# Performance work log

Hardware: AMD Instinct MI355X
Metric: run time of the kernel (lower is better)

Reference implementation:

```python
import jax, jax.numpy as jnp
import numpy as np

PATCH_NUMS = (1, 2, 4, 8, 16)
BETA = 0.25
A = -0.75  # torch bicubic coefficient


def _cubic(s):
    s = abs(s)
    if s <= 1.0:
        return ((A + 2.0) * s - (A + 3.0)) * s * s + 1.0
    if s < 2.0:
        return (((s - 5.0) * s + 8.0) * s - 4.0) * A
    return 0.0


def bicubic_matrix(n_in, n_out):
    # Row-stochastic 1D resampling matrix matching torch upsample_bicubic2d
    # (align_corners=False: half-pixel centers, border index clamping).
    scale = n_in / n_out
    W = np.zeros((n_out, n_in), dtype=np.float32)
    for i in range(n_out):
        x = (i + 0.5) * scale - 0.5
        x0 = int(np.floor(x))
        t = x - x0
        for off in (-1, 0, 1, 2):
            idx = min(max(x0 + off, 0), n_in - 1)
            W[i, idx] += _cubic(t - off)
    return jnp.asarray(W)


def area_down(x, pn):
    # exact average pooling (h, w divisible by pn)
    b, c, h, w = x.shape
    kh, kw = h // pn, w // pn
    return x.reshape(b, c, pn, kh, pn, kw).mean(axis=(3, 5))


def bicubic_up(x, h_out, w_out):
    b, c, h_in, w_in = x.shape
    Wh = bicubic_matrix(h_in, h_out)  # (h_out, h_in)
    Ww = bicubic_matrix(w_in, w_out)  # (w_out, w_in)
    x = jnp.einsum('Oh,bchw->bcOw', Wh, x)
    x = jnp.einsum('Pw,bchw->bchP', Ww, x)
    return x


def vector_quantize(z, embed, beta):
    # z: (b,c,h,w); embed: (V,c)
    b, c, h, w = z.shape
    zf = z.transpose(0, 2, 3, 1).reshape(-1, c)  # (N,c)
    # squared L2 distances to codebook, (N,V)
    d = (zf * zf).sum(-1, keepdims=True) - 2.0 * zf @ embed.T + (embed * embed).sum(-1)
    idx = jnp.argmin(d, axis=1)  # (N,)
    zq = embed[idx].reshape(b, h, w, c).transpose(0, 3, 1, 2)
    sg = jax.lax.stop_gradient
    loss = beta * jnp.mean((sg(zq) - z) ** 2) + jnp.mean((zq - sg(z)) ** 2)
    zq_st = z + sg(zq - z)  # straight-through estimator
    return zq_st, idx.reshape(b, h, w), loss


def setup_inputs() -> dict:
    key = jax.random.key(0)
    k1, k2 = jax.random.split(key)
    z = jax.random.normal(k1, (256, 32, 16, 16), dtype=jnp.float32)
    embed = jax.random.normal(k2, (4096, 32), dtype=jnp.float32)
    return {"z": z, "embed": embed}


def reference(z, embed):
    b, c, h, w = z.shape
    f_rest = z
    f_hat = jnp.zeros_like(z)
    ms_idx = []
    vq_loss = jnp.float32(0.0)
    n = len(PATCH_NUMS)
    for i, pn in enumerate(PATCH_NUMS):
        z_scale = area_down(f_rest, pn) if i < n - 1 else f_rest
        z_q_scale, idx, loss_i = vector_quantize(z_scale, embed, BETA)
        z_q = bicubic_up(z_q_scale, h, w) if i < n - 1 else z_q_scale
        f_hat = f_hat + z_q
        f_rest = f_rest - z_q
        ms_idx.append(idx)
        vq_loss = vq_loss + loss_i
    vq_loss = vq_loss / n
    return (f_hat, *ms_idx, vq_loss)
```

## Files before the change

kernel.cpp:

```cpp
#include <hip/hip_runtime.h>
#include <hip/hip_bf16.h>
#include <cstdint>
#include <cstddef>


#define B_   256
#define V_   4096
#define NTOT 2097152
#define WIN  128
#define CAP  768

using bf16x8 = __attribute__((ext_vector_type(8))) short;
using f32x4  = __attribute__((ext_vector_type(4))) float;

__device__ inline short f2bf(float f) {
  __hip_bfloat16 h = __float2bfloat16(f);
  return *reinterpret_cast<short*>(&h);
}
__device__ inline unsigned encf(float f) {
  unsigned u = __float_as_uint(f);
  return (u & 0x80000000u) ? ~u : (u | 0x80000000u);
}
__device__ inline float decf(unsigned u) {
  unsigned b = (u & 0x80000000u) ? (u ^ 0x80000000u) : ~u;
  return __uint_as_float(b);
}
__device__ inline int keyidx(unsigned long long k) {
  int i = (int)(unsigned)(k & 0xffffffffull);
  return min(max(i, 0), V_ - 1);
}

__global__ __launch_bounds__(256) void setup_kernel(
    const float* __restrict__ z, const float* __restrict__ embed,
    float* __restrict__ f_rest, float* __restrict__ f_hat,
    float* __restrict__ zpack, short* __restrict__ ebf,
    float* __restrict__ se, float* __restrict__ tables,
    float* __restrict__ loss_slots, unsigned long long* __restrict__ keys0,
    unsigned int* __restrict__ smin0)
{
  const int tid = threadIdx.x;
  const int t = blockIdx.x * 256 + tid;
  float v = z[t];
  f_rest[t] = v;
  f_hat[t] = 0.f;

  __shared__ float sm[256];
  sm[tid] = v;
  __syncthreads();
  if (tid == 0) {
    float s = 0.f;
    for (int i = 0; i < 256; ++i) s += sm[i];
    zpack[blockIdx.x] = s * (1.0f / 256.0f);
  }

  if (blockIdx.x < 16) {
    int code = blockIdx.x * 256 + tid;
    float s = 0.f;
#pragma unroll
    for (int c = 0; c < 32; ++c) {
      float e = embed[(size_t)code * 32 + c];
      ebf[(size_t)code * 32 + c] = f2bf(e);
      s += e * e;
    }
    se[code] = s;
  } else if (blockIdx.x == 16) {
    if (tid < 64) {
      int pn_i = tid >> 4;
      int o    = tid & 15;
      int pn   = 1 << pn_i;
      double scale = (double)pn / 16.0;
      double x  = (o + 0.5) * scale - 0.5;
      double x0 = floor(x);
      double tf = x - x0;
      float row[8];
#pragma unroll
      for (int h = 0; h < 8; ++h) row[h] = 0.f;
      const double A = -0.75;
#pragma unroll
      for (int off = -1; off <= 2; ++off) {
        double s = fabs(tf - (double)off);
        double cub;
        if (s <= 1.0)      cub = ((A + 2.0) * s - (A + 3.0)) * s * s + 1.0;
        else if (s < 2.0)  cub = (((s - 5.0) * s + 8.0) * s - 4.0) * A;
        else               cub = 0.0;
        int idx = (int)x0 + off;
        idx = min(max(idx, 0), pn - 1);
        row[idx] = (float)((double)row[idx] + cub);
      }
#pragma unroll
      for (int h = 0; h < 8; ++h) tables[pn_i * 128 + o * 8 + h] = row[h];
    }
  } else if (blockIdx.x == 17) {
    keys0[tid] = ~0ull;
    smin0[tid] = 0xFFFFFFFFu;
  } else if (blockIdx.x >= 20 && blockIdx.x < 60) {
    loss_slots[(blockIdx.x - 20) * 256 + tid] = 0.f;
  }
}

__global__ __launch_bounds__(256) void vq_phaseA_kernel(
    const float* __restrict__ zpack, const short* __restrict__ ebf,
    const float* __restrict__ se, unsigned int* __restrict__ smin,
    int vchunk)
{
  __shared__ __align__(16) short elds[WIN * 40];
  __shared__ float selds[WIN];

  const int tid = threadIdx.x;
  const int lane = tid & 63, wave = tid >> 6;
  const int col = lane & 15, quad = lane >> 4;
  const int nw = blockIdx.x * 256 + wave * 64;
  const int vbase = blockIdx.y * vchunk;

  bf16x8 af[4];
#pragma unroll
  for (int f = 0; f < 4; ++f) {
    const float* zr = zpack + (size_t)(nw + f * 16 + col) * 32 + quad * 8;
    float4 x = *(const float4*)zr;
    float4 y = *(const float4*)(zr + 4);
    af[f] = bf16x8{f2bf(-x.x), f2bf(-x.y), f2bf(-x.z), f2bf(-x.w),
                   f2bf(-y.x), f2bf(-y.y), f2bf(-y.z), f2bf(-y.w)};
  }
  float mn[4][4];
#pragma unroll
  for (int f = 0; f < 4; ++f)
#pragma unroll
    for (int r = 0; r < 4; ++r) mn[f][r] = 3.4e38f;

  for (int w0 = 0; w0 < vchunk; w0 += WIN) {
    __syncthreads();
    {
      int row = tid >> 1, half = tid & 1;
      const bf16x8* src = (const bf16x8*)(ebf + (size_t)(vbase + w0 + row) * 32);
      bf16x8* dst = (bf16x8*)(elds + row * 40);
      dst[half * 2]     = src[half * 2];
      dst[half * 2 + 1] = src[half * 2 + 1];
      if (tid < WIN) selds[tid] = 0.5f * se[vbase + w0 + tid];
    }
    __syncthreads();
    for (int vv = 0; vv < WIN; vv += 16) {
      bf16x8 bf = *(const bf16x8*)(elds + (vv + col) * 40 + quad * 8);
      float sevh = selds[vv + col];
      f32x4 cin = {sevh, sevh, sevh, sevh};
#pragma unroll
      for (int f = 0; f < 4; ++f) {
        f32x4 d = __builtin_amdgcn_mfma_f32_16x16x32_bf16(af[f], bf, cin, 0, 0, 0);
#pragma unroll
        for (int r = 0; r < 4; ++r) mn[f][r] = fminf(mn[f][r], d[r]);
      }
    }
  }
#pragma unroll
  for (int f = 0; f < 4; ++f)
#pragma unroll
    for (int r = 0; r < 4; ++r) {
      float m = mn[f][r];
      m = fminf(m, __shfl_xor(m, 1, 64));
      m = fminf(m, __shfl_xor(m, 2, 64));
      m = fminf(m, __shfl_xor(m, 4, 64));
      m = fminf(m, __shfl_xor(m, 8, 64));
      mn[f][r] = m;
    }
  if (col == 0) {
#pragma unroll
    for (int f = 0; f < 4; ++f)
#pragma unroll
      for (int r = 0; r < 4; ++r)
        atomicMin(&smin[nw + f * 16 + quad * 4 + r], encf(mn[f][r]));
  }
}

__global__ __launch_bounds__(256) void vq_phaseB_kernel(
    const float* __restrict__ zpack, const short* __restrict__ ebf,
    const float* __restrict__ se, const unsigned int* __restrict__ smin,
    const float* __restrict__ embed, unsigned long long* __restrict__ keys,
    int vchunk, int nmax)
{
  __shared__ __align__(16) short elds[WIN * 40];
  __shared__ float selds[WIN];
  __shared__ unsigned long long clist[CAP];
  __shared__ int ccnt;

  const int tid = threadIdx.x;
  const int lane = tid & 63, wave = tid >> 6;
  const int col = lane & 15, quad = lane >> 4;
  const int nw = blockIdx.x * 256 + wave * 64;
  const int vbase = blockIdx.y * vchunk;
  const float MARGIN = 1.0f;

  if (tid == 0) ccnt = 0;
  __syncthreads();

  bf16x8 af[4];
#pragma unroll
  for (int f = 0; f < 4; ++f) {
    const float* zr = zpack + (size_t)(nw + f * 16 + col) * 32 + quad * 8;
    float4 x = *(const float4*)zr;
    float4 y = *(const float4*)(zr + 4);
    af[f] = bf16x8{f2bf(-x.x), f2bf(-x.y), f2bf(-x.z), f2bf(-x.w),
                   f2bf(-y.x), f2bf(-y.y), f2bf(-y.z), f2bf(-y.w)};
  }
  float thr[4][4];
#pragma unroll
  for (int f = 0; f < 4; ++f)
#pragma unroll
    for (int r = 0; r < 4; ++r)
      thr[f][r] = decf(smin[nw + f * 16 + quad * 4 + r]) + MARGIN;

  for (int w0 = 0; w0 < vchunk; w0 += WIN) {
    __syncthreads();
    {
      int row = tid >> 1, half = tid & 1;
      const bf16x8* src = (const bf16x8*)(ebf + (size_t)(vbase + w0 + row) * 32);
      bf16x8* dst = (bf16x8*)(elds + row * 40);
      dst[half * 2]     = src[half * 2];
      dst[half * 2 + 1] = src[half * 2 + 1];
      if (tid < WIN) selds[tid] = 0.5f * se[vbase + w0 + tid];
    }
    __syncthreads();
    for (int vv = 0; vv < WIN; vv += 16) {
      bf16x8 bf = *(const bf16x8*)(elds + (vv + col) * 40 + quad * 8);
      float sevh = selds[vv + col];
      f32x4 cin = {sevh, sevh, sevh, sevh};
      f32x4 dd[4];
      float hm = 3.4e38f;
#pragma unroll
      for (int f = 0; f < 4; ++f) {
        dd[f] = __builtin_amdgcn_mfma_f32_16x16x32_bf16(af[f], bf, cin, 0, 0, 0);
#pragma unroll
        for (int r = 0; r < 4; ++r) hm = fminf(hm, dd[f][r] - thr[f][r]);
      }
      if (hm <= 0.f) {
#pragma unroll
        for (int f = 0; f < 4; ++f) {
#pragma unroll
          for (int r = 0; r < 4; ++r) {
            if (dd[f][r] <= thr[f][r]) {
              int n = nw + f * 16 + quad * 4 + r;
              int v = vbase + w0 + vv + col;
              int slot = atomicAdd(&ccnt, 1);
              if (slot < CAP) {
                clist[slot] =
                    ((unsigned long long)(unsigned)n << 32) | (unsigned)v;
              } else {
                const float* zp = zpack + (size_t)n * 32;
                const float* ep = embed + (size_t)v * 32;
                float dot = 0.f, sz = 0.f;
#pragma unroll 1
                for (int i = 0; i < 8; ++i) {
                  float4 z4 = *(const float4*)(zp + 4 * i);
                  float4 e4 = *(const float4*)(ep + 4 * i);
                  dot = fmaf(z4.x, e4.x, dot); dot = fmaf(z4.y, e4.y, dot);
                  dot = fmaf(z4.z, e4.z, dot); dot = fmaf(z4.w, e4.w, dot);
                  sz  = fmaf(z4.x, z4.x, sz);  sz  = fmaf(z4.y, z4.y, sz);
                  sz  = fmaf(z4.z, z4.z, sz);  sz  = fmaf(z4.w, z4.w, sz);
                }
                float d = fmaf(-2.0f, dot, sz) + se[v];
                unsigned long long key =
                    ((unsigned long long)encf(d) << 32) | (unsigned)v;
                atomicMin(&keys[n], key);
              }
            }
          }
        }
      }
    }
  }

  __syncthreads();
  int tot = min(ccnt, CAP);
  for (int j = tid; j < tot; j += 256) {
    unsigned long long cv = clist[j];
    int n = min((int)(cv >> 32), nmax - 1);
    int v = min((int)(cv & 0xffffffffull), V_ - 1);
    const float* zp = zpack + (size_t)n * 32;
    const float* ep = embed + (size_t)v * 32;
    float dot = 0.f, sz = 0.f;
#pragma unroll
    for (int i = 0; i < 8; ++i) {
      float4 z4 = *(const float4*)(zp + 4 * i);
      float4 e4 = *(const float4*)(ep + 4 * i);
      dot = fmaf(z4.x, e4.x, dot); dot = fmaf(z4.y, e4.y, dot);
      dot = fmaf(z4.z, e4.z, dot); dot = fmaf(z4.w, e4.w, dot);
      sz  = fmaf(z4.x, z4.x, sz);  sz  = fmaf(z4.y, z4.y, sz);
      sz  = fmaf(z4.z, z4.z, sz);  sz  = fmaf(z4.w, z4.w, sz);
    }
    float d = fmaf(-2.0f, dot, sz) + se[v];
    unsigned long long key =
        ((unsigned long long)encf(d) << 32) | (unsigned)v;
    atomicMin(&keys[n], key);
  }
}

__global__ __launch_bounds__(256) void up_update_kernel(
    const float* __restrict__ embed, const unsigned long long* __restrict__ keys,
    const float* __restrict__ tbl, float* __restrict__ f_hat,
    float* __restrict__ f_rest, int pn,
    float* __restrict__ zpack_next, unsigned long long* __restrict__ keys_nb,
    unsigned int* __restrict__ smin_nb, int pn_next, int n_next,
    float* __restrict__ idx_out, float* __restrict__ loss_slot)
{
  __shared__ float sm[256];
  __shared__ float sm_e[64];
  const int tid = threadIdx.x;
  const int t = blockIdx.x * 256 + tid;
  const int p = tid & 15, o = tid >> 4;
  const int c = blockIdx.x & 31, b = blockIdx.x >> 5;
  const int pn2 = pn * pn;

  float pre = f_rest[t];
  sm[tid] = pre;
  if (tid < pn2) {
    int idx = keyidx(keys[b * pn2 + tid]);
    if (c == 0) idx_out[b * pn2 + tid] = (float)idx;
    sm_e[tid] = embed[(size_t)idx * 32 + c];
  }
  __syncthreads();

  float lsum = 0.f;
  if (tid < pn2) {
    int k = 16 / pn;
    int ph = tid / pn, pw = tid - ph * pn;
    float s = 0.f;
    for (int i = 0; i < k; ++i)
      for (int j = 0; j < k; ++j)
        s += sm[(ph * k + i) * 16 + (pw * k + j)];
    float zavg = s * (1.0f / (k * k));
    float d = sm_e[tid] - zavg;
    lsum = d * d;
  }
#pragma unroll
  for (int off = 32; off > 0; off >>= 1) lsum += __shfl_down(lsum, off, 64);
  if ((tid & 63) == 0)
    atomicAdd(loss_slot + ((blockIdx.x & 127) << 4), lsum);

  const float* Wo = tbl + o * 8;
  const float* Wp = tbl + p * 8;
  float acc = 0.f;
  for (int w = 0; w < pn; ++w) {
    float inner = 0.f;
    for (int h = 0; h < pn; ++h)
      inner = fmaf(Wo[h], sm_e[h * pn + w], inner);
    acc = fmaf(Wp[w], inner, acc);
  }
  float nr = pre - acc;
  f_hat[t] += acc;
  f_rest[t] = nr;

  __syncthreads();
  sm[tid] = nr;
  __syncthreads();
  const int pnn2 = pn_next * pn_next;
  if (tid < pnn2) {
    int ph = tid / pn_next, pw = tid - ph * pn_next;
    int k = 16 / pn_next;
    float s = 0.f;
    for (int i = 0; i < k; ++i)
      for (int j = 0; j < k; ++j)
        s += sm[(ph * k + i) * 16 + (pw * k + j)];
    int n = b * pnn2 + ph * pn_next + pw;
    zpack_next[(size_t)n * 32 + c] = s * (1.0f / (k * k));
  }
  if (t < n_next) {
    keys_nb[t] = ~0ull;
    smin_nb[t] = 0xFFFFFFFFu;
  }
}

__global__ __launch_bounds__(256) void final_add_kernel(
    const float* __restrict__ embed, const unsigned long long* __restrict__ keys,
    float* __restrict__ f_hat, const float* __restrict__ zpack,
    float* __restrict__ idx_out, float* __restrict__ loss_slot)
{
  const int tid = threadIdx.x;
  const int t = blockIdx.x * 256 + tid;
  const int c = blockIdx.x & 31, b = blockIdx.x >> 5;
  const int n = b * 256 + tid;
  int idx = keyidx(keys[n]);
  if (c == 0) idx_out[n] = (float)idx;
  float e = embed[(size_t)idx * 32 + c];
  f_hat[t] += e;
  float d = e - zpack[(size_t)n * 32 + c];
  float lsum = d * d;
#pragma unroll
  for (int off = 32; off > 0; off >>= 1) lsum += __shfl_down(lsum, off, 64);
  if ((tid & 63) == 0)
    atomicAdd(loss_slot + ((blockIdx.x & 127) << 4), lsum);
}

__global__ __launch_bounds__(128) void loss_final_kernel(
    const float* __restrict__ loss_slots, float* __restrict__ out_loss)
{
  __shared__ float lred[2];
  const int tid = threadIdx.x;
  const float numel[5] = {8192.f, 32768.f, 131072.f, 524288.f, 2097152.f};
  float tot = 0.f;
  for (int s = 0; s < 5; ++s) {
    float x = loss_slots[s * 2048 + tid * 16];
#pragma unroll
    for (int off = 32; off > 0; off >>= 1) x += __shfl_down(x, off, 64);
    if ((tid & 63) == 0) lred[tid >> 6] = x;
    __syncthreads();
    if (tid == 0) {
      float m = (lred[0] + lred[1]) / numel[s];
      tot += 0.25f * m + m;
    }
    __syncthreads();
  }
  if (tid == 0) out_loss[0] = tot / 5.f;
}

extern "C" void kernel_launch(void* const* d_in, const int* in_sizes, int n_in,
                              void* d_out, int out_size, void* d_ws, size_t ws_size,
                              hipStream_t stream)
{
  const float* z     = (const float*)d_in[0];
  const float* embed = (const float*)d_in[1];
  float* out = (float*)d_out;
  float* ws  = (float*)d_ws;

  float* f_rest = ws;
  float* zpack  = ws + 2097152;
  short* ebf    = (short*)(ws + 4194304);
  float* se     = ws + 4259840;
  unsigned int* smin0 = (unsigned int*)(ws + 4263936);
  unsigned int* smin1 = (unsigned int*)(ws + 4329472);
  unsigned long long* keys0 = (unsigned long long*)(ws + 4345856);
  unsigned long long* keys1 = (unsigned long long*)(ws + 4476928);
  float* loss_slots = ws + 4509696;
  float* tables     = ws + 4519936;

  unsigned long long* keysb[2] = {keys0, keys1};
  unsigned int*       sminb[2] = {smin0, smin1};

  setup_kernel<<<NTOT / 256, 256, 0, stream>>>(z, embed, f_rest, out, zpack,
                                               ebf, se, tables, loss_slots,
                                               keys0, smin0);

  const int PN[5]  = {1, 2, 4, 8, 16};
  const int NVC[5] = {32, 32, 32, 16, 16};
  int idx_off = NTOT;
  for (int i = 0; i < 5; ++i) {
    int pn = PN[i];
    int N  = B_ * pn * pn;
    int vchunk = V_ / NVC[i];
    unsigned long long* kb = keysb[i & 1];
    unsigned int*       sb = sminb[i & 1];
    dim3 g(N / 256, NVC[i]);
    vq_phaseA_kernel<<<g, 256, 0, stream>>>(zpack, ebf, se, sb, vchunk);
    vq_phaseB_kernel<<<g, 256, 0, stream>>>(zpack, ebf, se, sb, embed, kb,
                                            vchunk, N);
    if (i < 4) {
      int pnn = PN[i + 1];
      up_update_kernel<<<NTOT / 256, 256, 0, stream>>>(
          embed, kb, tables + i * 128, out, f_rest, pn,
          zpack, keysb[(i + 1) & 1], sminb[(i + 1) & 1],
          pnn, B_ * pnn * pnn, out + idx_off, loss_slots + i * 2048);
    } else {
      final_add_kernel<<<NTOT / 256, 256, 0, stream>>>(
          embed, kb, out, zpack, out + idx_off, loss_slots + 4 * 2048);
    }
    idx_off += N;
  }
  loss_final_kernel<<<1, 128, 0, stream>>>(loss_slots, out + 2184448);
}
```

Baseline: 426.5 us.

## Transpose zpack to channel-major layout and derive f_hat from z minus f_rest

Stores the packed per-scale vectors channel-major (c*65536 + n) so the writes from up_update and setup become coalesced across threads, while the VQ kernels gather strided scalars. It also drops the running f_hat accumulation in setup and every up_update pass, and computes f_hat once at the end as z - f_rest + e, removing a read-modify-write of the full tensor per scale. The risks are uncoalesced strided loads in the VQ fragment loads and candidate rescoring, and slightly different float rounding for f_hat.

```diff
diff --git a/kernel.cpp b/kernel.cpp
--- a/kernel.cpp
+++ b/kernel.cpp
@@ -9,6 +9,7 @@
 #define NTOT 2097152
 #define WIN  128
 #define CAP  768
+#define ZS   65536
 
 using bf16x8 = __attribute__((ext_vector_type(8))) short;
 using f32x4  = __attribute__((ext_vector_type(4))) float;
@@ -32,17 +33,15 @@
 
 __global__ __launch_bounds__(256) void setup_kernel(
     const float* __restrict__ z, const float* __restrict__ embed,
-    float* __restrict__ f_rest, float* __restrict__ f_hat,
-    float* __restrict__ zpack, short* __restrict__ ebf,
-    float* __restrict__ se, float* __restrict__ tables,
-    float* __restrict__ loss_slots, unsigned long long* __restrict__ keys0,
-    unsigned int* __restrict__ smin0)
+    float* __restrict__ f_rest, float* __restrict__ zpack,
+    short* __restrict__ ebf, float* __restrict__ se,
+    float* __restrict__ tables, float* __restrict__ loss_slots,
+    unsigned long long* __restrict__ keys0, unsigned int* __restrict__ smin0)
 {
   const int tid = threadIdx.x;
   const int t = blockIdx.x * 256 + tid;
   float v = z[t];
   f_rest[t] = v;
-  f_hat[t] = 0.f;
 
   __shared__ float sm[256];
   sm[tid] = v;
@@ -50,7 +49,8 @@
   if (tid == 0) {
     float s = 0.f;
     for (int i = 0; i < 256; ++i) s += sm[i];
-    zpack[blockIdx.x] = s * (1.0f / 256.0f);
+    int c = blockIdx.x & 31, b = blockIdx.x >> 5;
+    zpack[c * ZS + b] = s * (1.0f / 256.0f);
   }
 
   if (blockIdx.x < 16) {
@@ -115,11 +115,10 @@
   bf16x8 af[4];
 #pragma unroll
   for (int f = 0; f < 4; ++f) {
-    const float* zr = zpack + (size_t)(nw + f * 16 + col) * 32 + quad * 8;
-    float4 x = *(const float4*)zr;
-    float4 y = *(const float4*)(zr + 4);
-    af[f] = bf16x8{f2bf(-x.x), f2bf(-x.y), f2bf(-x.z), f2bf(-x.w),
-                   f2bf(-y.x), f2bf(-y.y), f2bf(-y.z), f2bf(-y.w)};
+    const float* zb = zpack + (nw + f * 16 + col);
+#pragma unroll
+    for (int j = 0; j < 8; ++j)
+      af[f][j] = f2bf(-zb[(size_t)(quad * 8 + j) * ZS]);
   }
   float mn[4][4];
 #pragma unroll
@@ -194,11 +193,10 @@
   bf16x8 af[4];
 #pragma unroll
   for (int f = 0; f < 4; ++f) {
-    const float* zr = zpack + (size_t)(nw + f * 16 + col) * 32 + quad * 8;
-    float4 x = *(const float4*)zr;
-    float4 y = *(const float4*)(zr + 4);
-    af[f] = bf16x8{f2bf(-x.x), f2bf(-x.y), f2bf(-x.z), f2bf(-x.w),
-                   f2bf(-y.x), f2bf(-y.y), f2bf(-y.z), f2bf(-y.w)};
+    const float* zb = zpack + (nw + f * 16 + col);
+#pragma unroll
+    for (int j = 0; j < 8; ++j)
+      af[f][j] = f2bf(-zb[(size_t)(quad * 8 + j) * ZS]);
   }
   float thr[4][4];
 #pragma unroll
@@ -243,17 +241,14 @@
                 clist[slot] =
                     ((unsigned long long)(unsigned)n << 32) | (unsigned)v;
               } else {
-                const float* zp = zpack + (size_t)n * 32;
+                const float* zp = zpack + n;
                 const float* ep = embed + (size_t)v * 32;
                 float dot = 0.f, sz = 0.f;
 #pragma unroll 1
-                for (int i = 0; i < 8; ++i) {
-                  float4 z4 = *(const float4*)(zp + 4 * i);
-                  float4 e4 = *(const float4*)(ep + 4 * i);
-                  dot = fmaf(z4.x, e4.x, dot); dot = fmaf(z4.y, e4.y, dot);
-                  dot = fmaf(z4.z, e4.z, dot); dot = fmaf(z4.w, e4.w, dot);
-                  sz  = fmaf(z4.x, z4.x, sz);  sz  = fmaf(z4.y, z4.y, sz);
-                  sz  = fmaf(z4.z, z4.z, sz);  sz  = fmaf(z4.w, z4.w, sz);
+                for (int i = 0; i < 32; ++i) {
+                  float zc = zp[(size_t)i * ZS];
+                  dot = fmaf(zc, ep[i], dot);
+                  sz  = fmaf(zc, zc, sz);
                 }
                 float d = fmaf(-2.0f, dot, sz) + se[v];
                 unsigned long long key =
@@ -273,17 +268,14 @@
     unsigned long long cv = clist[j];
     int n = min((int)(cv >> 32), nmax - 1);
     int v = min((int)(cv & 0xffffffffull), V_ - 1);
-    const float* zp = zpack + (size_t)n * 32;
+    const float* zp = zpack + n;
     const float* ep = embed + (size_t)v * 32;
     float dot = 0.f, sz = 0.f;
 #pragma unroll
-    for (int i = 0; i < 8; ++i) {
-      float4 z4 = *(const float4*)(zp + 4 * i);
-      float4 e4 = *(const float4*)(ep + 4 * i);
-      dot = fmaf(z4.x, e4.x, dot); dot = fmaf(z4.y, e4.y, dot);
-      dot = fmaf(z4.z, e4.z, dot); dot = fmaf(z4.w, e4.w, dot);
-      sz  = fmaf(z4.x, z4.x, sz);  sz  = fmaf(z4.y, z4.y, sz);
-      sz  = fmaf(z4.z, z4.z, sz);  sz  = fmaf(z4.w, z4.w, sz);
+    for (int i = 0; i < 32; ++i) {
+      float zc = zp[(size_t)i * ZS];
+      dot = fmaf(zc, ep[i], dot);
+      sz  = fmaf(zc, zc, sz);
     }
     float d = fmaf(-2.0f, dot, sz) + se[v];
     unsigned long long key =
@@ -294,8 +286,7 @@
 
 __global__ __launch_bounds__(256) void up_update_kernel(
     const float* __restrict__ embed, const unsigned long long* __restrict__ keys,
-    const float* __restrict__ tbl, float* __restrict__ f_hat,
-    float* __restrict__ f_rest, int pn,
+    const float* __restrict__ tbl, float* __restrict__ f_rest, int pn,
     float* __restrict__ zpack_next, unsigned long long* __restrict__ keys_nb,
     unsigned int* __restrict__ smin_nb, int pn_next, int n_next,
     float* __restrict__ idx_out, float* __restrict__ loss_slot)
@@ -344,7 +335,6 @@
     acc = fmaf(Wp[w], inner, acc);
   }
   float nr = pre - acc;
-  f_hat[t] += acc;
   f_rest[t] = nr;
 
   __syncthreads();
@@ -358,8 +348,7 @@
     for (int i = 0; i < k; ++i)
       for (int j = 0; j < k; ++j)
         s += sm[(ph * k + i) * 16 + (pw * k + j)];
-    int n = b * pnn2 + ph * pn_next + pw;
-    zpack_next[(size_t)n * 32 + c] = s * (1.0f / (k * k));
+    zpack_next[c * ZS + b * pnn2 + tid] = s * (1.0f / (k * k));
   }
   if (t < n_next) {
     keys_nb[t] = ~0ull;
@@ -368,6 +357,7 @@
 }
 
 __global__ __launch_bounds__(256) void final_add_kernel(
+    const float* __restrict__ z, const float* __restrict__ f_rest,
     const float* __restrict__ embed, const unsigned long long* __restrict__ keys,
     float* __restrict__ f_hat, const float* __restrict__ zpack,
     float* __restrict__ idx_out, float* __restrict__ loss_slot)
@@ -379,8 +369,8 @@
   int idx = keyidx(keys[n]);
   if (c == 0) idx_out[n] = (float)idx;
   float e = embed[(size_t)idx * 32 + c];
-  f_hat[t] += e;
-  float d = e - zpack[(size_t)n * 32 + c];
+  f_hat[t] = (z[t] - f_rest[t]) + e;
+  float d = e - zpack[c * ZS + n];
   float lsum = d * d;
 #pragma unroll
   for (int off = 32; off > 0; off >>= 1) lsum += __shfl_down(lsum, off, 64);
@@ -433,7 +423,7 @@
   unsigned long long* keysb[2] = {keys0, keys1};
   unsigned int*       sminb[2] = {smin0, smin1};
 
-  setup_kernel<<<NTOT / 256, 256, 0, stream>>>(z, embed, f_rest, out, zpack,
+  setup_kernel<<<NTOT / 256, 256, 0, stream>>>(z, embed, f_rest, zpack,
                                                ebf, se, tables, loss_slots,
                                                keys0, smin0);
 
@@ -453,12 +443,13 @@
     if (i < 4) {
       int pnn = PN[i + 1];
       up_update_kernel<<<NTOT / 256, 256, 0, stream>>>(
-          embed, kb, tables + i * 128, out, f_rest, pn,
+          embed, kb, tables + i * 128, f_rest, pn,
           zpack, keysb[(i + 1) & 1], sminb[(i + 1) & 1],
           pnn, B_ * pnn * pnn, out + idx_off, loss_slots + i * 2048);
     } else {
       final_add_kernel<<<NTOT / 256, 256, 0, stream>>>(
-          embed, kb, out, zpack, out + idx_off, loss_slots + 4 * 2048);
+          z, f_rest, embed, kb, out, zpack, out + idx_off,
+          loss_slots + 4 * 2048);
     }
     idx_off += N;
   }
```

Result: faster. 402.8 us (-5.6%).
